# Optimization experiments

Measured on AMD Instinct MI355X. Metric: run time of the kernel, lower is better.

## Reference

```python
import jax, jax.numpy as jnp
import numpy as np

BN_EPS = 1e-5


def _batchnorm(x, gamma, beta):
    # training-mode BatchNorm2d: biased batch stats over (N, H, W)
    mean = jnp.mean(x, axis=(0, 2, 3), keepdims=True)
    var = jnp.var(x, axis=(0, 2, 3), keepdims=True)
    xn = (x - mean) * jax.lax.rsqrt(var + BN_EPS)
    return xn * gamma[None, :, None, None] + beta[None, :, None, None]


def _bin_weight(w):
    # BitConv2d_Robust: w_bin = sign(w) * mean(|w|) per output channel (STE in fwd is just the value)
    alpha = jnp.mean(jnp.abs(w), axis=(1, 2, 3), keepdims=True)
    return jax.lax.stop_gradient(jnp.sign(w) * alpha - w) + w


def _conv(x, w, b, pad):
    y = jax.lax.conv_general_dilated(
        x, w, window_strides=(1, 1), padding=[(pad, pad), (pad, pad)],
        dimension_numbers=('NCHW', 'OIHW', 'NCHW'))
    return y + b[None, :, None, None]


def setup_inputs() -> dict:
    key = jax.random.key(0)
    ks = jax.random.split(key, 14)
    B, Cin, Cout, T, H, W = 16, 128, 256, 512, 64, 64
    fan1 = Cin * 9
    fan2 = Cout * 9
    return {
        'x': jax.random.normal(ks[0], (B, Cin, H, W), jnp.float32),
        't': jax.random.normal(ks[1], (B, T), jnp.float32),
        'bn1_g': jnp.ones((Cin,), jnp.float32),
        'bn1_b': jnp.zeros((Cin,), jnp.float32),
        'w1': jax.random.normal(ks[2], (Cout, Cin, 3, 3), jnp.float32) / np.sqrt(fan1),
        'b1': jax.random.normal(ks[3], (Cout,), jnp.float32) * 0.01,
        'tW': jax.random.normal(ks[4], (Cout, T), jnp.float32) / np.sqrt(T),
        'tb': jax.random.normal(ks[5], (Cout,), jnp.float32) * 0.01,
        'bn2_g': jnp.ones((Cout,), jnp.float32),
        'bn2_b': jnp.zeros((Cout,), jnp.float32),
        'w2': jax.random.normal(ks[6], (Cout, Cout, 3, 3), jnp.float32) / np.sqrt(fan2),
        'b2': jax.random.normal(ks[7], (Cout,), jnp.float32) * 0.01,
        'ws': jax.random.normal(ks[8], (Cout, Cin, 1, 1), jnp.float32) / np.sqrt(Cin),
        'bs': jax.random.normal(ks[9], (Cout,), jnp.float32) * 0.01,
    }


def reference(x, t, bn1_g, bn1_b, w1, b1, tW, tb, bn2_g, bn2_b, w2, b2, ws, bs):
    h = jnp.sign(_batchnorm(x, bn1_g, bn1_b))                # BN + sign binarize
    h = _conv(h, _bin_weight(w1), b1, pad=1)                  # binarized 3x3 conv
    temb = t @ tW.T + tb                                      # time MLP -> [B, Cout]
    h = h + temb[:, :, None, None]
    h = jnp.sign(_batchnorm(h, bn2_g, bn2_b))
    h = _conv(h, _bin_weight(w2), b2, pad=1)
    skip = _conv(x, _bin_weight(ws), bs, pad=0)               # 1x1 binarized skip (in_ch != out_ch)
    return h + skip
```

## Files before the change

### kernel.cpp

```cpp
#include <hip/hip_runtime.h>
#include <stdint.h>

typedef unsigned int uint;
typedef short bf16x8 __attribute__((ext_vector_type(8)));
typedef float f32x4 __attribute__((ext_vector_type(4)));

#define EPS 1e-5f


__global__ __launch_bounds__(256) void k_bn1_part(const float* __restrict__ x, float* __restrict__ part) {
  int c = blockIdx.x, chunk = blockIdx.y;
  float s = 0.f, s2 = 0.f;
  #pragma unroll
  for (int jb = 0; jb < 2; ++jb) {
    int b = chunk * 2 + jb;
    const float4* xb = (const float4*)(x + (((size_t)((b << 7) | c)) << 12));
    #pragma unroll
    for (int k = 0; k < 4; ++k) {
      float4 q = xb[k * 256 + threadIdx.x];
      s += (q.x + q.y) + (q.z + q.w);
      s2 += q.x * q.x + q.y * q.y + q.z * q.z + q.w * q.w;
    }
  }
  #pragma unroll
  for (int off = 32; off > 0; off >>= 1) { s += __shfl_down(s, off); s2 += __shfl_down(s2, off); }
  __shared__ float ls[4], ls2[4];
  int wid = threadIdx.x >> 6, lane = threadIdx.x & 63;
  if (lane == 0) { ls[wid] = s; ls2[wid] = s2; }
  __syncthreads();
  if (threadIdx.x == 0) {
    part[(c * 8 + chunk) * 2 + 0] = ls[0] + ls[1] + ls[2] + ls[3];
    part[(c * 8 + chunk) * 2 + 1] = ls2[0] + ls2[1] + ls2[2] + ls2[3];
  }
}

__global__ void k_bn1_fin(const float* __restrict__ part, const float* __restrict__ g,
                          const float* __restrict__ be, float* __restrict__ sc, float* __restrict__ sh) {
  int c = threadIdx.x;
  float s = 0.f, s2 = 0.f;
  for (int k = 0; k < 8; ++k) { s += part[(c * 8 + k) * 2]; s2 += part[(c * 8 + k) * 2 + 1]; }
  const float inv = 1.f / 65536.f;
  float m = s * inv, var = s2 * inv - m * m;
  float rs = rsqrtf(var + EPS);
  float scale = rs * g[c];
  sc[c] = scale;
  sh[c] = be[c] - m * scale;
}

__global__ __launch_bounds__(128) void k_packw1(const float* __restrict__ w1, uint* __restrict__ wb,
                                                float* __restrict__ alpha) {
  int co = blockIdx.x, wid = threadIdx.x >> 6, lane = threadIdx.x & 63;
  const float* wp = w1 + (co * 128 + threadIdx.x) * 9;
  float wv[9]; float s = 0.f;
  #pragma unroll
  for (int tp = 0; tp < 9; ++tp) { wv[tp] = wp[tp]; s += fabsf(wv[tp]); }
  #pragma unroll
  for (int tp = 0; tp < 9; ++tp) {
    unsigned long long m = __ballot(wv[tp] > 0.f);
    if (lane == 0) {
      wb[(co * 9 + tp) * 4 + wid * 2 + 0] = (uint)m;
      wb[(co * 9 + tp) * 4 + wid * 2 + 1] = (uint)(m >> 32);
    }
  }
  #pragma unroll
  for (int off = 32; off > 0; off >>= 1) s += __shfl_down(s, off);
  __shared__ float l2[2];
  if (lane == 0) l2[wid] = s;
  __syncthreads();
  if (threadIdx.x == 0) alpha[co] = (l2[0] + l2[1]) * (1.f / 1152.f);
}

__global__ __launch_bounds__(256) void k_packw2(const float* __restrict__ w2, uint* __restrict__ wb,
                                                float* __restrict__ alpha, ushort* __restrict__ wT) {
  int co = blockIdx.x, wid = threadIdx.x >> 6, lane = threadIdx.x & 63;
  int ci = threadIdx.x;
  const float* wp = w2 + (co * 256 + ci) * 9;
  float wv[9]; float s = 0.f;
  #pragma unroll
  for (int tp = 0; tp < 9; ++tp) { wv[tp] = wp[tp]; s += fabsf(wv[tp]); }
  int chunk = ci >> 7, kc = (ci >> 5) & 3, cil = ci & 31;
  #pragma unroll
  for (int tp = 0; tp < 9; ++tp) {
    wT[(((tp << 3) + (chunk << 2) + kc) << 13) + (co << 5) + cil] = (wv[tp] > 0.f) ? 0x3F80u : 0xBF80u;
    unsigned long long m = __ballot(wv[tp] > 0.f);
    if (lane == 0) {
      wb[(co * 9 + tp) * 8 + wid * 2 + 0] = (uint)m;
      wb[(co * 9 + tp) * 8 + wid * 2 + 1] = (uint)(m >> 32);
    }
  }
  #pragma unroll
  for (int off = 32; off > 0; off >>= 1) s += __shfl_down(s, off);
  __shared__ float l4[4];
  if (lane == 0) l4[wid] = s;
  __syncthreads();
  if (threadIdx.x == 0) alpha[co] = (l4[0] + l4[1] + l4[2] + l4[3]) * (1.f / 2304.f);
}

__global__ __launch_bounds__(256) void k_base(const uint* __restrict__ wb1, const uint* __restrict__ wb2,
                                              int* __restrict__ base1, int* __restrict__ base2) {
  int co = threadIdx.x;
  int pc1[9], pc2[9];
  #pragma unroll
  for (int tp = 0; tp < 9; ++tp) {
    uint a = 0;
    #pragma unroll
    for (int k = 0; k < 4; ++k) a += __popc(wb1[co * 36 + tp * 4 + k]);
    pc1[tp] = (int)a;
    uint b = 0;
    #pragma unroll
    for (int k = 0; k < 8; ++k) b += __popc(wb2[co * 72 + tp * 8 + k]);
    pc2[tp] = (int)b;
  }
  #pragma unroll
  for (int pat = 0; pat < 9; ++pat) {
    int yt = pat / 3, xt = pat % 3;
    int b1v = 1152, b2v = 2304;
    #pragma unroll
    for (int tp = 0; tp < 9; ++tp) {
      int dy = tp / 3 - 1, dx = tp % 3 - 1;
      bool inv = (dy < 0 && yt == 0) || (dy > 0 && yt == 2) || (dx < 0 && xt == 0) || (dx > 0 && xt == 2);
      if (inv) { b1v -= 128 - 2 * pc1[tp]; b2v -= 256 - 2 * pc2[tp]; }
    }
    base1[pat * 256 + co] = b1v;
    base2[pat * 256 + co] = b2v;
  }
}

__global__ __launch_bounds__(128) void k_packws(const float* __restrict__ wsk, float* __restrict__ swT) {
  int co = blockIdx.x, ci = threadIdx.x;
  float v = wsk[co * 128 + ci];
  float s = fabsf(v);
  #pragma unroll
  for (int off = 32; off > 0; off >>= 1) s += __shfl_down(s, off);
  __shared__ float l2[2]; __shared__ float tot;
  int wid = threadIdx.x >> 6, lane = threadIdx.x & 63;
  if (lane == 0) l2[wid] = s;
  __syncthreads();
  if (threadIdx.x == 0) tot = (l2[0] + l2[1]) * (1.f / 128.f);
  __syncthreads();
  float a = tot;
  swT[ci * 256 + co] = (v > 0.f) ? a : -a;
}

__global__ __launch_bounds__(256) void k_temb(const float* __restrict__ t, const float* __restrict__ tW,
                                              const float* __restrict__ tbias, float* __restrict__ temb) {
  int b = blockIdx.x, co = threadIdx.x;
  const float* tr = t + b * 512;
  const float* wr = tW + co * 512;
  float a0 = 0, a1 = 0, a2 = 0, a3 = 0;
  #pragma unroll 8
  for (int k = 0; k < 512; k += 4) {
    a0 = fmaf(tr[k + 0], wr[k + 0], a0);
    a1 = fmaf(tr[k + 1], wr[k + 1], a1);
    a2 = fmaf(tr[k + 2], wr[k + 2], a2);
    a3 = fmaf(tr[k + 3], wr[k + 3], a3);
  }
  temb[b * 256 + co] = (a0 + a1) + (a2 + a3) + tbias[co];
}

__global__ __launch_bounds__(256, 2) void k_skip(const float* __restrict__ x, const float* __restrict__ swT,
                                                 const float* __restrict__ bsk, const float* __restrict__ b2,
                                                 const float* __restrict__ sc1, const float* __restrict__ sh1,
                                                 uint* __restrict__ sbinw, float* __restrict__ out) {
  __shared__ float xs[128 * 64];
  __shared__ float wsl[128 * 64];
  int g = blockIdx.x;
  int b = g >> 6;
  int px0 = (g & 63) << 6;
  int co0 = blockIdx.y << 6;
  int t = threadIdx.x;

  {
    const float* xb = x + ((size_t)(b << 7) << 12) + px0;
    float4* xs4 = (float4*)xs;
    #pragma unroll
    for (int k = 0; k < 8; ++k) {
      int idx = k * 256 + t;
      int ci = idx >> 4, f4 = idx & 15;
      xs4[idx] = *(const float4*)(xb + ((size_t)ci << 12) + (f4 << 2));
    }
  }
  {
    float4* ws4 = (float4*)wsl;
    #pragma unroll
    for (int k = 0; k < 8; ++k) {
      int idx = k * 256 + t;
      int ci = idx >> 4, f4 = idx & 15;
      ws4[idx] = *(const float4*)(swT + ci * 256 + co0 + (f4 << 2));
    }
  }
  __syncthreads();

  if (blockIdx.y == 0) {
    int px = t & 63, wd = t >> 6;
    int ci0 = wd << 5;
    uint acc = 0;
    #pragma unroll
    for (int i = 0; i < 32; ++i) {
      int ci = ci0 + i;
      float v = xs[ci * 64 + px];
      acc |= ((v * sc1[ci] + sh1[ci]) > 0.f ? 1u : 0u) << i;
    }
    sbinw[(((size_t)b << 12) | (px0 + px)) * 4 + wd] = acc;
  }

  int tx = t & 15, ty = t >> 4;
  const float4* xs4 = (const float4*)xs;
  const float4* ws4 = (const float4*)wsl;
  float4 acc0 = make_float4(0, 0, 0, 0), acc1 = acc0, acc2 = acc0, acc3 = acc0;
  #pragma unroll 4
  for (int ci = 0; ci < 128; ++ci) {
    float4 xv = xs4[ci * 16 + tx];
    float4 wv = ws4[ci * 16 + ty];
    acc0.x = fmaf(wv.x, xv.x, acc0.x); acc0.y = fmaf(wv.x, xv.y, acc0.y);
    acc0.z = fmaf(wv.x, xv.z, acc0.z); acc0.w = fmaf(wv.x, xv.w, acc0.w);
    acc1.x = fmaf(wv.y, xv.x, acc1.x); acc1.y = fmaf(wv.y, xv.y, acc1.y);
    acc1.z = fmaf(wv.y, xv.z, acc1.z); acc1.w = fmaf(wv.y, xv.w, acc1.w);
    acc2.x = fmaf(wv.z, xv.x, acc2.x); acc2.y = fmaf(wv.z, xv.y, acc2.y);
    acc2.z = fmaf(wv.z, xv.z, acc2.z); acc2.w = fmaf(wv.z, xv.w, acc2.w);
    acc3.x = fmaf(wv.w, xv.x, acc3.x); acc3.y = fmaf(wv.w, xv.y, acc3.y);
    acc3.z = fmaf(wv.w, xv.z, acc3.z); acc3.w = fmaf(wv.w, xv.w, acc3.w);
  }

  float* op = out + ((size_t)b << 20) + px0 + (tx << 2);
  int cob = co0 + (ty << 2);
  float4 r;
  r = acc0; { float bb = bsk[cob + 0] + b2[cob + 0]; r.x += bb; r.y += bb; r.z += bb; r.w += bb; }
  *(float4*)(op + (size_t)(cob + 0) * 4096) = r;
  r = acc1; { float bb = bsk[cob + 1] + b2[cob + 1]; r.x += bb; r.y += bb; r.z += bb; r.w += bb; }
  *(float4*)(op + (size_t)(cob + 1) * 4096) = r;
  r = acc2; { float bb = bsk[cob + 2] + b2[cob + 2]; r.x += bb; r.y += bb; r.z += bb; r.w += bb; }
  *(float4*)(op + (size_t)(cob + 2) * 4096) = r;
  r = acc3; { float bb = bsk[cob + 3] + b2[cob + 3]; r.x += bb; r.y += bb; r.z += bb; r.w += bb; }
  *(float4*)(op + (size_t)(cob + 3) * 4096) = r;
}

__global__ __launch_bounds__(256, 1) void k_conv1(const uint4* __restrict__ sbin, const uint* __restrict__ wb1,
                                                  const int* __restrict__ base1, short* __restrict__ S1) {
  __shared__ uint wlds[32 * 36];
  __shared__ int blds[9 * 32];
  int co0 = blockIdx.y << 5;
  #pragma unroll
  for (int k = 0; k < 4; ++k) wlds[k * 256 + threadIdx.x] = wb1[co0 * 36 + k * 256 + threadIdx.x];
  if (threadIdx.x < 128) wlds[1024 + threadIdx.x] = wb1[co0 * 36 + 1024 + threadIdx.x];
  #pragma unroll
  for (int k = 0; k < 2; ++k) {
    int idx = k * 256 + threadIdx.x;
    if (idx < 288) blds[idx] = base1[(idx >> 5) * 256 + co0 + (idx & 31)];
  }

  int bt = blockIdx.x;
  int b = bt >> 4;
  int y = ((bt & 15) << 2) | (threadIdx.x >> 6);
  int cx = threadIdx.x & 63;
  uint nb[9][4];
  #pragma unroll
  for (int dy = -1; dy <= 1; ++dy)
    #pragma unroll
    for (int dx = -1; dx <= 1; ++dx) {
      int tp = (dy + 1) * 3 + (dx + 1);
      int yy = y + dy, xx = cx + dx;
      bool v = ((unsigned)yy < 64u) && ((unsigned)xx < 64u);
      uint4 q = make_uint4(0, 0, 0, 0);
      if (v) q = sbin[(b << 12) | (yy << 6) | xx];
      nb[tp][0] = q.x; nb[tp][1] = q.y; nb[tp][2] = q.z; nb[tp][3] = q.w;
    }
  int pat = ((y == 0) ? 0 : ((y == 63) ? 6 : 3)) + ((cx == 0) ? 0 : ((cx == 63) ? 2 : 1));
  __syncthreads();

  int p = (y << 6) | cx;
  short* op = S1 + ((size_t)b << 20) + ((size_t)co0 << 12) + p;
  #pragma unroll 1
  for (int cc = 0; cc < 4; ++cc) {
    short accv[8];
    #pragma unroll
    for (int j = 0; j < 8; ++j) {
      int co_l = cc * 8 + j;
      const uint4* wp4 = (const uint4*)(wlds + co_l * 36);
      uint m0 = 0, m1 = 0, m2 = 0, m3 = 0;
      #pragma unroll
      for (int tp = 0; tp < 9; ++tp) {
        uint4 w4 = wp4[tp];
        m0 += __popc(nb[tp][0] ^ w4.x);
        m1 += __popc(nb[tp][1] ^ w4.y);
        m2 += __popc(nb[tp][2] ^ w4.z);
        m3 += __popc(nb[tp][3] ^ w4.w);
      }
      accv[j] = (short)(blds[pat * 32 + co_l] - 2 * (int)((m0 + m1) + (m2 + m3)));
    }
    #pragma unroll
    for (int j = 0; j < 8; ++j) op[(size_t)(cc * 8 + j) << 12] = accv[j];
  }
}

__global__ __launch_bounds__(256) void k_bn2_part(const short* __restrict__ S1, const float* __restrict__ al1,
                                                  const float* __restrict__ b1, const float* __restrict__ temb,
                                                  float* __restrict__ part) {
  int co = blockIdx.x, chunk = blockIdx.y;
  float a = al1[co], bb = b1[co];
  float s = 0.f, s2 = 0.f;
  #pragma unroll
  for (int jb = 0; jb < 2; ++jb) {
    int b = chunk * 2 + jb;
    float tb_ = bb + temb[(b << 8) | co];
    const uint4* sp = (const uint4*)(S1 + ((size_t)b << 20) + ((size_t)co << 12));
    #pragma unroll
    for (int k = 0; k < 2; ++k) {
      uint4 q = sp[k * 256 + threadIdx.x];
      uint ws[4] = {q.x, q.y, q.z, q.w};
      #pragma unroll
      for (int w = 0; w < 4; ++w) {
        float f0 = fmaf(a, (float)((short)(ws[w] & 0xffffu)), tb_);
        float f1 = fmaf(a, (float)((short)(ws[w] >> 16)), tb_);
        s += f0 + f1;
        s2 += f0 * f0 + f1 * f1;
      }
    }
  }
  #pragma unroll
  for (int off = 32; off > 0; off >>= 1) { s += __shfl_down(s, off); s2 += __shfl_down(s2, off); }
  __shared__ float ls[4], ls2[4];
  int wid = threadIdx.x >> 6, lane = threadIdx.x & 63;
  if (lane == 0) { ls[wid] = s; ls2[wid] = s2; }
  __syncthreads();
  if (threadIdx.x == 0) {
    part[(co * 8 + chunk) * 2 + 0] = ls[0] + ls[1] + ls[2] + ls[3];
    part[(co * 8 + chunk) * 2 + 1] = ls2[0] + ls2[1] + ls2[2] + ls2[3];
  }
}

__global__ void k_bn2_fin(const float* __restrict__ part, const float* __restrict__ al1,
                          const float* __restrict__ b1, const float* __restrict__ g2,
                          const float* __restrict__ be2, float* __restrict__ A,
                          float* __restrict__ Bc, float* __restrict__ Cc) {
  int co = threadIdx.x;
  float s = 0.f, s2 = 0.f;
  for (int k = 0; k < 8; ++k) { s += part[(co * 8 + k) * 2]; s2 += part[(co * 8 + k) * 2 + 1]; }
  const float inv = 1.f / 65536.f;
  float m = s * inv, var = s2 * inv - m * m;
  float rs = rsqrtf(var + EPS);
  float gg = rs * g2[co];
  A[co] = al1[co] * gg;
  Bc[co] = (b1[co] - m) * gg + be2[co];
  Cc[co] = gg;
}

__global__ __launch_bounds__(256) void k_bin2_bf16(const short* __restrict__ S1, const float* __restrict__ A,
                                                   const float* __restrict__ Bc, const float* __restrict__ Cc,
                                                   const float* __restrict__ temb, uint4* __restrict__ h2u4) {
  __shared__ uint4 tile[64 * 32];
  int b = blockIdx.x >> 6;
  int px0 = (blockIdx.x & 63) << 6;
  int pxl = threadIdx.x & 63, quad = threadIdx.x >> 6;
  const short* sp = S1 + ((size_t)b << 20) + (px0 + pxl);
  const float* tp = temb + (b << 8);
  #pragma unroll 1
  for (int g = 0; g < 8; ++g) {
    uint d[4];
    #pragma unroll
    for (int h = 0; h < 4; ++h) {
      int c0 = quad * 64 + g * 8 + h * 2;
      float v0 = A[c0] * (float)sp[(size_t)c0 << 12] + Bc[c0] + Cc[c0] * tp[c0];
      float v1 = A[c0 + 1] * (float)sp[(size_t)(c0 + 1) << 12] + Bc[c0 + 1] + Cc[c0 + 1] * tp[c0 + 1];
      uint s0 = (v0 > 0.f) ? 0x3F80u : 0xBF80u;
      uint s1 = (v1 > 0.f) ? 0x3F80u : 0xBF80u;
      d[h] = s0 | (s1 << 16);
    }
    int slot = quad * 8 + g;
    tile[pxl * 32 + (slot ^ (pxl & 7))] = make_uint4(d[0], d[1], d[2], d[3]);
  }
  __syncthreads();
  uint4* dst = h2u4 + ((size_t)(b << 12) + px0) * 32;
  #pragma unroll
  for (int k = 0; k < 8; ++k) {
    int c = k * 256 + threadIdx.x;
    int px = c >> 5, slot = c & 31;
    dst[c] = tile[px * 32 + (slot ^ (px & 7))];
  }
}

__global__ __launch_bounds__(256, 2) void k_conv2_mfma(const ushort* __restrict__ h2,
                                                       const ushort* __restrict__ wT,
                                                       const float* __restrict__ al2,
                                                       float* __restrict__ out) {
  __shared__ ushort act[4 * 66 * 128];
  int bidx = blockIdx.x;
  int s = (bidx & 7) * 64 + (bidx >> 3);
  int b = s >> 5, y0 = (s & 31) << 1;
  int lane = threadIdx.x & 63, wave = threadIdx.x >> 6;
  int co0 = wave << 6;
  int l15 = lane & 15, lk = lane >> 4;

  f32x4 acc[4][8] = {};

  const uint4* h2g = (const uint4*)h2;
  uint4* a4 = (uint4*)act;
  const size_t abase = (size_t)((co0 + l15) << 5) + (lk << 3);

#define LOADAV(dst, ptr)                                                     \
  {                                                                          \
    _Pragma("unroll")                                                        \
    for (int ct_ = 0; ct_ < 4; ++ct_)                                        \
      dst[ct_] = *(const bf16x8*)((ptr) + abase + (ct_ << 9));               \
  }

#define KC_BLOCK(AV, kcv)                                                    \
  {                                                                          \
    _Pragma("unroll")                                                        \
    for (int r_ = 0; r_ < 2; ++r_) {                                         \
      bf16x8 Bv[4];                                                          \
      _Pragma("unroll")                                                      \
      for (int pt_ = 0; pt_ < 4; ++pt_) {                                    \
        int xi_ = (r_ + ty) * 66 + tx + pt_ * 16 + l15;                      \
        int u_ = (((xi_ << 4) + ((kcv) << 2) + lk) ^ (xi_ & 7));             \
        Bv[pt_] = *(bf16x8*)&act[u_ << 3];                                   \
      }                                                                      \
      _Pragma("unroll")                                                      \
      for (int ct_ = 0; ct_ < 4; ++ct_)                                      \
        _Pragma("unroll")                                                    \
        for (int pt_ = 0; pt_ < 4; ++pt_)                                    \
          acc[ct_][r_ * 4 + pt_] = __builtin_amdgcn_mfma_f32_16x16x32_bf16(  \
              AV[ct_], Bv[pt_], acc[ct_][r_ * 4 + pt_], 0, 0, 0);            \
    }                                                                        \
  }

  #pragma unroll 1
  for (int chunk = 0; chunk < 2; ++chunk) {
    if (chunk) __syncthreads();
    #pragma unroll 1
    for (int i = 0; i < 17; ++i) {
      int idx = i * 256 + threadIdx.x;
      if (idx < 4224) {
        int q = idx & 15, rowxz = idx >> 4;
        int xz = rowxz % 66, r = rowxz / 66;
        int yy = y0 + r - 1, xx = xz - 1;
        uint4 v = make_uint4(0, 0, 0, 0);
        if (((unsigned)yy < 64u) && ((unsigned)xx < 64u))
          v = h2g[(size_t)((b << 12) | (yy << 6) | xx) * 32 + chunk * 16 + q];
        a4[((rowxz << 4) + q) ^ (rowxz & 7)] = v;
      }
    }
    __syncthreads();

    const ushort* wch = wT + ((size_t)chunk << 15);
    bf16x8 AvA[4], AvB[4];
    LOADAV(AvA, wch);

    #pragma unroll 1
    for (int tp = 0; tp < 9; ++tp) {
      int ty = tp / 3, tx = tp % 3;
      const ushort* wtp = wch + ((size_t)tp << 16);
      const ushort* wnx = (tp < 8) ? (wtp + (1 << 16)) : wtp;

      LOADAV(AvB, wtp + (1 << 13));  KC_BLOCK(AvA, 0);
      LOADAV(AvA, wtp + (2 << 13));  KC_BLOCK(AvB, 1);
      LOADAV(AvB, wtp + (3 << 13));  KC_BLOCK(AvA, 2);
      LOADAV(AvA, wnx);              KC_BLOCK(AvB, 3);
    }
  }
#undef LOADAV
#undef KC_BLOCK

  #pragma unroll
  for (int ct = 0; ct < 4; ++ct) {
    #pragma unroll
    for (int r = 0; r < 2; ++r) {
      #pragma unroll
      for (int pt = 0; pt < 4; ++pt) {
        int x = pt * 16 + l15;
        float* ob = out + ((size_t)b << 20) + ((y0 + r) << 6) + x;
        #pragma unroll
        for (int j = 0; j < 4; ++j) {
          int co = co0 + ct * 16 + lk * 4 + j;
          float* p = ob + ((size_t)co << 12);
          *p = fmaf(al2[co], acc[ct][r * 4 + pt][j], *p);
        }
      }
    }
  }
}

__global__ __launch_bounds__(256) void k_bin2_packed(const short* __restrict__ S1, const float* __restrict__ A,
                                                     const float* __restrict__ Bc, const float* __restrict__ Cc,
                                                     const float* __restrict__ temb, uint4* __restrict__ hbin) {
  int pg = blockIdx.x * 256 + threadIdx.x;
  int b = pg >> 12, p = pg & 4095;
  int c0 = blockIdx.y << 7;
  const short* sp = S1 + ((size_t)b << 20) + p;
  const float* tp = temb + (b << 8);
  uint w[4];
  #pragma unroll
  for (int wd = 0; wd < 4; ++wd) {
    uint acc = 0;
    #pragma unroll
    for (int i = 0; i < 32; ++i) {
      int co = c0 + wd * 32 + i;
      float v = A[co] * (float)sp[(size_t)co << 12] + Bc[co] + Cc[co] * tp[co];
      acc |= (v > 0.f ? 1u : 0u) << i;
    }
    w[wd] = acc;
  }
  hbin[pg * 2 + blockIdx.y] = make_uint4(w[0], w[1], w[2], w[3]);
}

__global__ __launch_bounds__(256, 1) void k_conv2_pop(const uint4* __restrict__ hbin, const uint* __restrict__ wb2,
                                                      const int* __restrict__ base2, const float* __restrict__ al2,
                                                      float* __restrict__ out) {
  __shared__ uint wlds[32 * 72];
  __shared__ int blds[9 * 32];
  int co0 = blockIdx.y << 5;
  #pragma unroll
  for (int k = 0; k < 9; ++k) wlds[k * 256 + threadIdx.x] = wb2[co0 * 72 + k * 256 + threadIdx.x];
  #pragma unroll
  for (int k = 0; k < 2; ++k) {
    int idx = k * 256 + threadIdx.x;
    if (idx < 288) blds[idx] = base2[(idx >> 5) * 256 + co0 + (idx & 31)];
  }
  int bt = blockIdx.x;
  int b = bt >> 4;
  int y = ((bt & 15) << 2) | (threadIdx.x >> 6);
  int cx = threadIdx.x & 63;
  uint nb[9][8];
  #pragma unroll
  for (int dy = -1; dy <= 1; ++dy)
    #pragma unroll
    for (int dx = -1; dx <= 1; ++dx) {
      int tp = (dy + 1) * 3 + (dx + 1);
      int yy = y + dy, xx = cx + dx;
      bool v = ((unsigned)yy < 64u) && ((unsigned)xx < 64u);
      uint4 q0 = make_uint4(0, 0, 0, 0), q1 = make_uint4(0, 0, 0, 0);
      if (v) {
        int pix = (b << 12) | (yy << 6) | xx;
        q0 = hbin[pix * 2 + 0];
        q1 = hbin[pix * 2 + 1];
      }
      nb[tp][0] = q0.x; nb[tp][1] = q0.y; nb[tp][2] = q0.z; nb[tp][3] = q0.w;
      nb[tp][4] = q1.x; nb[tp][5] = q1.y; nb[tp][6] = q1.z; nb[tp][7] = q1.w;
    }
  int pat = ((y == 0) ? 0 : ((y == 63) ? 6 : 3)) + ((cx == 0) ? 0 : ((cx == 63) ? 2 : 1));
  __syncthreads();

  int p = (y << 6) | cx;
  float* op = out + ((size_t)b << 20) + ((size_t)co0 << 12) + p;
  #pragma unroll 1
  for (int cc = 0; cc < 4; ++cc) {
    float ov[8];
    #pragma unroll
    for (int j = 0; j < 8; ++j) ov[j] = op[(size_t)(cc * 8 + j) << 12];
    #pragma unroll
    for (int j = 0; j < 8; ++j) {
      int co_l = cc * 8 + j;
      const uint4* wp4 = (const uint4*)(wlds + co_l * 72);
      uint m0 = 0, m1 = 0, m2 = 0, m3 = 0;
      #pragma unroll
      for (int tp = 0; tp < 9; ++tp) {
        uint4 wa = wp4[tp * 2 + 0];
        uint4 wb_ = wp4[tp * 2 + 1];
        m0 += __popc(nb[tp][0] ^ wa.x);
        m1 += __popc(nb[tp][1] ^ wa.y);
        m2 += __popc(nb[tp][2] ^ wa.z);
        m3 += __popc(nb[tp][3] ^ wa.w);
        m0 += __popc(nb[tp][4] ^ wb_.x);
        m1 += __popc(nb[tp][5] ^ wb_.y);
        m2 += __popc(nb[tp][6] ^ wb_.z);
        m3 += __popc(nb[tp][7] ^ wb_.w);
      }
      int acc = blds[pat * 32 + co_l] - 2 * (int)((m0 + m1) + (m2 + m3));
      ov[j] = fmaf(al2[co0 + co_l], (float)acc, ov[j]);
    }
    #pragma unroll
    for (int j = 0; j < 8; ++j) op[(size_t)(cc * 8 + j) << 12] = ov[j];
  }
}

extern "C" void kernel_launch(void* const* d_in, const int* in_sizes, int n_in,
                              void* d_out, int out_size, void* d_ws, size_t ws_size,
                              hipStream_t stream) {
  const float* x    = (const float*)d_in[0];
  const float* t    = (const float*)d_in[1];
  const float* bn1g = (const float*)d_in[2];
  const float* bn1b = (const float*)d_in[3];
  const float* w1   = (const float*)d_in[4];
  const float* b1   = (const float*)d_in[5];
  const float* tW   = (const float*)d_in[6];
  const float* tb   = (const float*)d_in[7];
  const float* bn2g = (const float*)d_in[8];
  const float* bn2b = (const float*)d_in[9];
  const float* w2   = (const float*)d_in[10];
  const float* b2   = (const float*)d_in[11];
  const float* wsk  = (const float*)d_in[12];
  const float* bsk  = (const float*)d_in[13];
  float* out = (float*)d_out;
  char* ws = (char*)d_ws;

  float* bn1part = (float*)(ws + 0);
  float* sc1     = (float*)(ws + 8192);
  float* sh1     = (float*)(ws + 8704);
  uint4* sbin    = (uint4*)(ws + 9216);
  uint*  wb1     = (uint*) (ws + 1057792);
  float* al1     = (float*)(ws + 1094656);
  uint*  wb2     = (uint*) (ws + 1095680);
  float* al2     = (float*)(ws + 1169408);
  float* swkT    = (float*)(ws + 1170432);
  float* temb    = (float*)(ws + 1301504);
  float* bn2part = (float*)(ws + 1317888);
  float* A2      = (float*)(ws + 1334272);
  float* Bc2     = (float*)(ws + 1335296);
  float* Cc2     = (float*)(ws + 1336320);
  int*   base1g  = (int*)  (ws + 1337344);
  int*   base2g  = (int*)  (ws + 1346560);
  uint4* hbin    = (uint4*)(ws + 1355776);
  ushort* wT2    = (ushort*)(ws + 3452928);
  short* S1      = (short*)(ws + 4632576);
  ushort* h2     = (ushort*)(ws + 38187008);
  const size_t WS_NEED_MFMA = 71741440ULL;
  bool use_mfma = (ws_size >= WS_NEED_MFMA);

  k_bn1_part<<<dim3(128, 8), 256, 0, stream>>>(x, bn1part);
  k_bn1_fin<<<1, 128, 0, stream>>>(bn1part, bn1g, bn1b, sc1, sh1);
  k_packw1<<<256, 128, 0, stream>>>(w1, wb1, al1);
  k_packw2<<<256, 256, 0, stream>>>(w2, wb2, al2, wT2);
  k_base<<<1, 256, 0, stream>>>(wb1, wb2, base1g, base2g);
  k_packws<<<256, 128, 0, stream>>>(wsk, swkT);
  k_temb<<<16, 256, 0, stream>>>(t, tW, tb, temb);
  k_skip<<<dim3(1024, 4), 256, 0, stream>>>(x, swkT, bsk, b2, sc1, sh1, (uint*)sbin, out);
  k_conv1<<<dim3(256, 8), 256, 0, stream>>>(sbin, wb1, base1g, S1);
  k_bn2_part<<<dim3(256, 8), 256, 0, stream>>>(S1, al1, b1, temb, bn2part);
  k_bn2_fin<<<1, 256, 0, stream>>>(bn2part, al1, b1, bn2g, bn2b, A2, Bc2, Cc2);
  if (use_mfma) {
    k_bin2_bf16<<<1024, 256, 0, stream>>>(S1, A2, Bc2, Cc2, temb, (uint4*)h2);
    k_conv2_mfma<<<512, 256, 0, stream>>>(h2, wT2, al2, out);
  } else {
    k_bin2_packed<<<dim3(256, 2), 256, 0, stream>>>(S1, A2, Bc2, Cc2, temb, hbin);
    k_conv2_pop<<<dim3(256, 8), 256, 0, stream>>>(hbin, wb2, base2g, al2, out);
  }
}
```

Baseline: 240.2 us.

## Run conv1 on bf16 MFMA with fused BN2 partial statistics

```diff
diff --git a/kernel.cpp b/kernel.cpp
--- a/kernel.cpp
+++ b/kernel.cpp
@@ -48,14 +48,16 @@
 }
 
 __global__ __launch_bounds__(128) void k_packw1(const float* __restrict__ w1, uint* __restrict__ wb,
-                                                float* __restrict__ alpha) {
+                                                float* __restrict__ alpha, ushort* __restrict__ wT1) {
   int co = blockIdx.x, wid = threadIdx.x >> 6, lane = threadIdx.x & 63;
-  const float* wp = w1 + (co * 128 + threadIdx.x) * 9;
+  int ci = threadIdx.x;
+  const float* wp = w1 + (co * 128 + ci) * 9;
   float wv[9]; float s = 0.f;
   #pragma unroll
   for (int tp = 0; tp < 9; ++tp) { wv[tp] = wp[tp]; s += fabsf(wv[tp]); }
   #pragma unroll
   for (int tp = 0; tp < 9; ++tp) {
+    wT1[(((tp << 2) + (ci >> 5)) << 13) + (co << 5) + (ci & 31)] = (wv[tp] > 0.f) ? 0x3F80u : 0xBF80u;
     unsigned long long m = __ballot(wv[tp] > 0.f);
     if (lane == 0) {
       wb[(co * 9 + tp) * 4 + wid * 2 + 0] = (uint)m;
@@ -161,7 +163,8 @@
 __global__ __launch_bounds__(256, 2) void k_skip(const float* __restrict__ x, const float* __restrict__ swT,
                                                  const float* __restrict__ bsk, const float* __restrict__ b2,
                                                  const float* __restrict__ sc1, const float* __restrict__ sh1,
-                                                 uint* __restrict__ sbinw, float* __restrict__ out) {
+                                                 uint* __restrict__ sbinw, ushort* __restrict__ h1w,
+                                                 int mfma1, float* __restrict__ out) {
   __shared__ float xs[128 * 64];
   __shared__ float wsl[128 * 64];
   int g = blockIdx.x;
@@ -194,14 +197,27 @@
   if (blockIdx.y == 0) {
     int px = t & 63, wd = t >> 6;
     int ci0 = wd << 5;
-    uint acc = 0;
-    #pragma unroll
-    for (int i = 0; i < 32; ++i) {
-      int ci = ci0 + i;
-      float v = xs[ci * 64 + px];
-      acc |= ((v * sc1[ci] + sh1[ci]) > 0.f ? 1u : 0u) << i;
-    }
-    sbinw[(((size_t)b << 12) | (px0 + px)) * 4 + wd] = acc;
+    if (mfma1) {
+      ushort hv[32];
+      #pragma unroll
+      for (int i = 0; i < 32; ++i) {
+        int ci = ci0 + i;
+        float v = xs[ci * 64 + px];
+        hv[i] = ((v * sc1[ci] + sh1[ci]) > 0.f) ? (ushort)0x3F80u : (ushort)0xBF80u;
+      }
+      uint4* dst = (uint4*)(h1w + (((size_t)((b << 12) | (px0 + px))) << 7) + (wd << 5));
+      const uint4* src = (const uint4*)hv;
+      dst[0] = src[0]; dst[1] = src[1]; dst[2] = src[2]; dst[3] = src[3];
+    } else {
+      uint acc = 0;
+      #pragma unroll
+      for (int i = 0; i < 32; ++i) {
+        int ci = ci0 + i;
+        float v = xs[ci * 64 + px];
+        acc |= ((v * sc1[ci] + sh1[ci]) > 0.f ? 1u : 0u) << i;
+      }
+      sbinw[(((size_t)b << 12) | (px0 + px)) * 4 + wd] = acc;
+    }
   }
 
   int tx = t & 15, ty = t >> 4;
@@ -235,154 +251,11 @@
   *(float4*)(op + (size_t)(cob + 3) * 4096) = r;
 }
 
-__global__ __launch_bounds__(256, 1) void k_conv1(const uint4* __restrict__ sbin, const uint* __restrict__ wb1,
-                                                  const int* __restrict__ base1, short* __restrict__ S1) {
-  __shared__ uint wlds[32 * 36];
-  __shared__ int blds[9 * 32];
-  int co0 = blockIdx.y << 5;
-  #pragma unroll
-  for (int k = 0; k < 4; ++k) wlds[k * 256 + threadIdx.x] = wb1[co0 * 36 + k * 256 + threadIdx.x];
-  if (threadIdx.x < 128) wlds[1024 + threadIdx.x] = wb1[co0 * 36 + 1024 + threadIdx.x];
-  #pragma unroll
-  for (int k = 0; k < 2; ++k) {
-    int idx = k * 256 + threadIdx.x;
-    if (idx < 288) blds[idx] = base1[(idx >> 5) * 256 + co0 + (idx & 31)];
-  }
-
-  int bt = blockIdx.x;
-  int b = bt >> 4;
-  int y = ((bt & 15) << 2) | (threadIdx.x >> 6);
-  int cx = threadIdx.x & 63;
-  uint nb[9][4];
-  #pragma unroll
-  for (int dy = -1; dy <= 1; ++dy)
-    #pragma unroll
-    for (int dx = -1; dx <= 1; ++dx) {
-      int tp = (dy + 1) * 3 + (dx + 1);
-      int yy = y + dy, xx = cx + dx;
-      bool v = ((unsigned)yy < 64u) && ((unsigned)xx < 64u);
-      uint4 q = make_uint4(0, 0, 0, 0);
-      if (v) q = sbin[(b << 12) | (yy << 6) | xx];
-      nb[tp][0] = q.x; nb[tp][1] = q.y; nb[tp][2] = q.z; nb[tp][3] = q.w;
-    }
-  int pat = ((y == 0) ? 0 : ((y == 63) ? 6 : 3)) + ((cx == 0) ? 0 : ((cx == 63) ? 2 : 1));
-  __syncthreads();
-
-  int p = (y << 6) | cx;
-  short* op = S1 + ((size_t)b << 20) + ((size_t)co0 << 12) + p;
-  #pragma unroll 1
-  for (int cc = 0; cc < 4; ++cc) {
-    short accv[8];
-    #pragma unroll
-    for (int j = 0; j < 8; ++j) {
-      int co_l = cc * 8 + j;
-      const uint4* wp4 = (const uint4*)(wlds + co_l * 36);
-      uint m0 = 0, m1 = 0, m2 = 0, m3 = 0;
-      #pragma unroll
-      for (int tp = 0; tp < 9; ++tp) {
-        uint4 w4 = wp4[tp];
-        m0 += __popc(nb[tp][0] ^ w4.x);
-        m1 += __popc(nb[tp][1] ^ w4.y);
-        m2 += __popc(nb[tp][2] ^ w4.z);
-        m3 += __popc(nb[tp][3] ^ w4.w);
-      }
-      accv[j] = (short)(blds[pat * 32 + co_l] - 2 * (int)((m0 + m1) + (m2 + m3)));
-    }
-    #pragma unroll
-    for (int j = 0; j < 8; ++j) op[(size_t)(cc * 8 + j) << 12] = accv[j];
-  }
-}
-
-__global__ __launch_bounds__(256) void k_bn2_part(const short* __restrict__ S1, const float* __restrict__ al1,
-                                                  const float* __restrict__ b1, const float* __restrict__ temb,
-                                                  float* __restrict__ part) {
-  int co = blockIdx.x, chunk = blockIdx.y;
-  float a = al1[co], bb = b1[co];
-  float s = 0.f, s2 = 0.f;
-  #pragma unroll
-  for (int jb = 0; jb < 2; ++jb) {
-    int b = chunk * 2 + jb;
-    float tb_ = bb + temb[(b << 8) | co];
-    const uint4* sp = (const uint4*)(S1 + ((size_t)b << 20) + ((size_t)co << 12));
-    #pragma unroll
-    for (int k = 0; k < 2; ++k) {
-      uint4 q = sp[k * 256 + threadIdx.x];
-      uint ws[4] = {q.x, q.y, q.z, q.w};
-      #pragma unroll
-      for (int w = 0; w < 4; ++w) {
-        float f0 = fmaf(a, (float)((short)(ws[w] & 0xffffu)), tb_);
-        float f1 = fmaf(a, (float)((short)(ws[w] >> 16)), tb_);
-        s += f0 + f1;
-        s2 += f0 * f0 + f1 * f1;
-      }
-    }
-  }
-  #pragma unroll
-  for (int off = 32; off > 0; off >>= 1) { s += __shfl_down(s, off); s2 += __shfl_down(s2, off); }
-  __shared__ float ls[4], ls2[4];
-  int wid = threadIdx.x >> 6, lane = threadIdx.x & 63;
-  if (lane == 0) { ls[wid] = s; ls2[wid] = s2; }
-  __syncthreads();
-  if (threadIdx.x == 0) {
-    part[(co * 8 + chunk) * 2 + 0] = ls[0] + ls[1] + ls[2] + ls[3];
-    part[(co * 8 + chunk) * 2 + 1] = ls2[0] + ls2[1] + ls2[2] + ls2[3];
-  }
-}
-
-__global__ void k_bn2_fin(const float* __restrict__ part, const float* __restrict__ al1,
-                          const float* __restrict__ b1, const float* __restrict__ g2,
-                          const float* __restrict__ be2, float* __restrict__ A,
-                          float* __restrict__ Bc, float* __restrict__ Cc) {
-  int co = threadIdx.x;
-  float s = 0.f, s2 = 0.f;
-  for (int k = 0; k < 8; ++k) { s += part[(co * 8 + k) * 2]; s2 += part[(co * 8 + k) * 2 + 1]; }
-  const float inv = 1.f / 65536.f;
-  float m = s * inv, var = s2 * inv - m * m;
-  float rs = rsqrtf(var + EPS);
-  float gg = rs * g2[co];
-  A[co] = al1[co] * gg;
-  Bc[co] = (b1[co] - m) * gg + be2[co];
-  Cc[co] = gg;
-}
-
-__global__ __launch_bounds__(256) void k_bin2_bf16(const short* __restrict__ S1, const float* __restrict__ A,
-                                                   const float* __restrict__ Bc, const float* __restrict__ Cc,
-                                                   const float* __restrict__ temb, uint4* __restrict__ h2u4) {
-  __shared__ uint4 tile[64 * 32];
-  int b = blockIdx.x >> 6;
-  int px0 = (blockIdx.x & 63) << 6;
-  int pxl = threadIdx.x & 63, quad = threadIdx.x >> 6;
-  const short* sp = S1 + ((size_t)b << 20) + (px0 + pxl);
-  const float* tp = temb + (b << 8);
-  #pragma unroll 1
-  for (int g = 0; g < 8; ++g) {
-    uint d[4];
-    #pragma unroll
-    for (int h = 0; h < 4; ++h) {
-      int c0 = quad * 64 + g * 8 + h * 2;
-      float v0 = A[c0] * (float)sp[(size_t)c0 << 12] + Bc[c0] + Cc[c0] * tp[c0];
-      float v1 = A[c0 + 1] * (float)sp[(size_t)(c0 + 1) << 12] + Bc[c0 + 1] + Cc[c0 + 1] * tp[c0 + 1];
-      uint s0 = (v0 > 0.f) ? 0x3F80u : 0xBF80u;
-      uint s1 = (v1 > 0.f) ? 0x3F80u : 0xBF80u;
-      d[h] = s0 | (s1 << 16);
-    }
-    int slot = quad * 8 + g;
-    tile[pxl * 32 + (slot ^ (pxl & 7))] = make_uint4(d[0], d[1], d[2], d[3]);
-  }
-  __syncthreads();
-  uint4* dst = h2u4 + ((size_t)(b << 12) + px0) * 32;
-  #pragma unroll
-  for (int k = 0; k < 8; ++k) {
-    int c = k * 256 + threadIdx.x;
-    int px = c >> 5, slot = c & 31;
-    dst[c] = tile[px * 32 + (slot ^ (px & 7))];
-  }
-}
-
-__global__ __launch_bounds__(256, 2) void k_conv2_mfma(const ushort* __restrict__ h2,
-                                                       const ushort* __restrict__ wT,
-                                                       const float* __restrict__ al2,
-                                                       float* __restrict__ out) {
+__global__ __launch_bounds__(256, 2) void k_conv1_mfma(const ushort* __restrict__ h1,
+                                                       const ushort* __restrict__ wT1,
+                                                       short* __restrict__ S1,
+                                                       float* __restrict__ part_s,
+                                                       float* __restrict__ part_s2) {
   __shared__ ushort act[4 * 66 * 128];
   int bidx = blockIdx.x;
   int s = (bidx & 7) * 64 + (bidx >> 3);
@@ -392,8 +265,7 @@
   int l15 = lane & 15, lk = lane >> 4;
 
   f32x4 acc[4][8] = {};
-
-  const uint4* h2g = (const uint4*)h2;
+  const uint4* h1g = (const uint4*)h1;
   uint4* a4 = (uint4*)act;
   const size_t abase = (size_t)((co0 + l15) << 5) + (lk << 3);
 
@@ -403,7 +275,6 @@
     for (int ct_ = 0; ct_ < 4; ++ct_)                                        \
       dst[ct_] = *(const bf16x8*)((ptr) + abase + (ct_ << 9));               \
   }
-
 #define KC_BLOCK(AV, kcv)                                                    \
   {                                                                          \
     _Pragma("unroll")                                                        \
@@ -425,6 +296,299 @@
   }
 
   #pragma unroll 1
+  for (int i = 0; i < 17; ++i) {
+    int idx = i * 256 + threadIdx.x;
+    if (idx < 4224) {
+      int q = idx & 15, rowxz = idx >> 4;
+      int xz = rowxz % 66, r = rowxz / 66;
+      int yy = y0 + r - 1, xx = xz - 1;
+      uint4 v = make_uint4(0, 0, 0, 0);
+      if (((unsigned)yy < 64u) && ((unsigned)xx < 64u))
+        v = h1g[(size_t)((b << 12) | (yy << 6) | xx) * 16 + q];
+      a4[((rowxz << 4) + q) ^ (rowxz & 7)] = v;
+    }
+  }
+  __syncthreads();
+
+  bf16x8 AvA[4], AvB[4];
+  LOADAV(AvA, wT1);
+  #pragma unroll 1
+  for (int tp = 0; tp < 9; ++tp) {
+    int ty = tp / 3, tx = tp % 3;
+    const ushort* wtp = wT1 + ((size_t)tp << 15);
+    const ushort* wnx = (tp < 8) ? (wtp + (1 << 15)) : wtp;
+
+    LOADAV(AvB, wtp + (1 << 13));  KC_BLOCK(AvA, 0);
+    LOADAV(AvA, wtp + (2 << 13));  KC_BLOCK(AvB, 1);
+    LOADAV(AvB, wtp + (3 << 13));  KC_BLOCK(AvA, 2);
+    LOADAV(AvA, wnx);              KC_BLOCK(AvB, 3);
+  }
+#undef LOADAV
+#undef KC_BLOCK
+
+  #pragma unroll
+  for (int ct = 0; ct < 4; ++ct)
+    #pragma unroll
+    for (int r = 0; r < 2; ++r)
+      #pragma unroll
+      for (int pt = 0; pt < 4; ++pt) {
+        int x = pt * 16 + l15;
+        short* ob = S1 + ((size_t)b << 20) + ((y0 + r) << 6) + x;
+        #pragma unroll
+        for (int j = 0; j < 4; ++j) {
+          int co = co0 + ct * 16 + lk * 4 + j;
+          ob[(size_t)co << 12] = (short)acc[ct][r * 4 + pt][j];
+        }
+      }
+  #pragma unroll
+  for (int ct = 0; ct < 4; ++ct) {
+    float s1v[4] = {0, 0, 0, 0}, s2v[4] = {0, 0, 0, 0};
+    #pragma unroll
+    for (int k = 0; k < 8; ++k)
+      #pragma unroll
+      for (int j = 0; j < 4; ++j) {
+        float v = acc[ct][k][j];
+        s1v[j] += v; s2v[j] += v * v;
+      }
+    #pragma unroll
+    for (int off = 1; off < 16; off <<= 1)
+      #pragma unroll
+      for (int j = 0; j < 4; ++j) {
+        s1v[j] += __shfl_xor(s1v[j], off);
+        s2v[j] += __shfl_xor(s2v[j], off);
+      }
+    if (l15 == 0) {
+      #pragma unroll
+      for (int j = 0; j < 4; ++j) {
+        int co = co0 + ct * 16 + lk * 4 + j;
+        part_s[(size_t)s * 256 + co] = s1v[j];
+        part_s2[(size_t)s * 256 + co] = s2v[j];
+      }
+    }
+  }
+}
+
+__global__ void k_bn2_fin2(const float* __restrict__ part_s, const float* __restrict__ part_s2,
+                           const float* __restrict__ al1, const float* __restrict__ b1,
+                           const float* __restrict__ g2, const float* __restrict__ be2,
+                           const float* __restrict__ temb,
+                           float* __restrict__ A, float* __restrict__ Bc, float* __restrict__ Cc) {
+  int co = blockIdx.x;
+  int t = threadIdx.x;
+  float sS = 0.f, scS = 0.f, s2 = 0.f;
+  for (int k = 0; k < 8; ++k) {
+    int blk = t + k * 64;
+    int b = blk >> 5;
+    float c = b1[co] + temb[(b << 8) + co];
+    float Sv = part_s[(size_t)blk * 256 + co];
+    sS += Sv; scS += c * Sv; s2 += part_s2[(size_t)blk * 256 + co];
+  }
+  #pragma unroll
+  for (int off = 32; off > 0; off >>= 1) {
+    sS += __shfl_down(sS, off); scS += __shfl_down(scS, off); s2 += __shfl_down(s2, off);
+  }
+  if (t == 0) {
+    float a = al1[co];
+    float sumc = 0.f, sumc2 = 0.f;
+    for (int b = 0; b < 16; ++b) { float c = b1[co] + temb[(b << 8) + co]; sumc += c; sumc2 += c * c; }
+    float sumY = a * sS + 4096.f * sumc;
+    float sumY2 = a * a * s2 + 2.f * a * scS + 4096.f * sumc2;
+    const float inv = 1.f / 65536.f;
+    float m = sumY * inv, var = sumY2 * inv - m * m;
+    float rs = rsqrtf(var + EPS);
+    float gg = rs * g2[co];
+    A[co] = a * gg;
+    Bc[co] = (b1[co] - m) * gg + be2[co];
+    Cc[co] = gg;
+  }
+}
+
+__global__ __launch_bounds__(256, 1) void k_conv1(const uint4* __restrict__ sbin, const uint* __restrict__ wb1,
+                                                  const int* __restrict__ base1, short* __restrict__ S1) {
+  __shared__ uint wlds[32 * 36];
+  __shared__ int blds[9 * 32];
+  int co0 = blockIdx.y << 5;
+  #pragma unroll
+  for (int k = 0; k < 4; ++k) wlds[k * 256 + threadIdx.x] = wb1[co0 * 36 + k * 256 + threadIdx.x];
+  if (threadIdx.x < 128) wlds[1024 + threadIdx.x] = wb1[co0 * 36 + 1024 + threadIdx.x];
+  #pragma unroll
+  for (int k = 0; k < 2; ++k) {
+    int idx = k * 256 + threadIdx.x;
+    if (idx < 288) blds[idx] = base1[(idx >> 5) * 256 + co0 + (idx & 31)];
+  }
+  int bt = blockIdx.x;
+  int b = bt >> 4;
+  int y = ((bt & 15) << 2) | (threadIdx.x >> 6);
+  int cx = threadIdx.x & 63;
+  uint nb[9][4];
+  #pragma unroll
+  for (int dy = -1; dy <= 1; ++dy)
+    #pragma unroll
+    for (int dx = -1; dx <= 1; ++dx) {
+      int tp = (dy + 1) * 3 + (dx + 1);
+      int yy = y + dy, xx = cx + dx;
+      bool v = ((unsigned)yy < 64u) && ((unsigned)xx < 64u);
+      uint4 q = make_uint4(0, 0, 0, 0);
+      if (v) q = sbin[(b << 12) | (yy << 6) | xx];
+      nb[tp][0] = q.x; nb[tp][1] = q.y; nb[tp][2] = q.z; nb[tp][3] = q.w;
+    }
+  int pat = ((y == 0) ? 0 : ((y == 63) ? 6 : 3)) + ((cx == 0) ? 0 : ((cx == 63) ? 2 : 1));
+  __syncthreads();
+  int p = (y << 6) | cx;
+  short* op = S1 + ((size_t)b << 20) + ((size_t)co0 << 12) + p;
+  #pragma unroll 1
+  for (int cc = 0; cc < 4; ++cc) {
+    short accv[8];
+    #pragma unroll
+    for (int j = 0; j < 8; ++j) {
+      int co_l = cc * 8 + j;
+      const uint4* wp4 = (const uint4*)(wlds + co_l * 36);
+      uint m0 = 0, m1 = 0, m2 = 0, m3 = 0;
+      #pragma unroll
+      for (int tp = 0; tp < 9; ++tp) {
+        uint4 w4 = wp4[tp];
+        m0 += __popc(nb[tp][0] ^ w4.x);
+        m1 += __popc(nb[tp][1] ^ w4.y);
+        m2 += __popc(nb[tp][2] ^ w4.z);
+        m3 += __popc(nb[tp][3] ^ w4.w);
+      }
+      accv[j] = (short)(blds[pat * 32 + co_l] - 2 * (int)((m0 + m1) + (m2 + m3)));
+    }
+    #pragma unroll
+    for (int j = 0; j < 8; ++j) op[(size_t)(cc * 8 + j) << 12] = accv[j];
+  }
+}
+
+__global__ __launch_bounds__(256) void k_bn2_part(const short* __restrict__ S1, const float* __restrict__ al1,
+                                                  const float* __restrict__ b1, const float* __restrict__ temb,
+                                                  float* __restrict__ part) {
+  int co = blockIdx.x, chunk = blockIdx.y;
+  float a = al1[co], bb = b1[co];
+  float s = 0.f, s2 = 0.f;
+  #pragma unroll
+  for (int jb = 0; jb < 2; ++jb) {
+    int b = chunk * 2 + jb;
+    float tb_ = bb + temb[(b << 8) | co];
+    const uint4* sp = (const uint4*)(S1 + ((size_t)b << 20) + ((size_t)co << 12));
+    #pragma unroll
+    for (int k = 0; k < 2; ++k) {
+      uint4 q = sp[k * 256 + threadIdx.x];
+      uint ws[4] = {q.x, q.y, q.z, q.w};
+      #pragma unroll
+      for (int w = 0; w < 4; ++w) {
+        float f0 = fmaf(a, (float)((short)(ws[w] & 0xffffu)), tb_);
+        float f1 = fmaf(a, (float)((short)(ws[w] >> 16)), tb_);
+        s += f0 + f1;
+        s2 += f0 * f0 + f1 * f1;
+      }
+    }
+  }
+  #pragma unroll
+  for (int off = 32; off > 0; off >>= 1) { s += __shfl_down(s, off); s2 += __shfl_down(s2, off); }
+  __shared__ float ls[4], ls2[4];
+  int wid = threadIdx.x >> 6, lane = threadIdx.x & 63;
+  if (lane == 0) { ls[wid] = s; ls2[wid] = s2; }
+  __syncthreads();
+  if (threadIdx.x == 0) {
+    part[(co * 8 + chunk) * 2 + 0] = ls[0] + ls[1] + ls[2] + ls[3];
+    part[(co * 8 + chunk) * 2 + 1] = ls2[0] + ls2[1] + ls2[2] + ls2[3];
+  }
+}
+
+__global__ void k_bn2_fin(const float* __restrict__ part, const float* __restrict__ al1,
+                          const float* __restrict__ b1, const float* __restrict__ g2,
+                          const float* __restrict__ be2, float* __restrict__ A,
+                          float* __restrict__ Bc, float* __restrict__ Cc) {
+  int co = threadIdx.x;
+  float s = 0.f, s2 = 0.f;
+  for (int k = 0; k < 8; ++k) { s += part[(co * 8 + k) * 2]; s2 += part[(co * 8 + k) * 2 + 1]; }
+  const float inv = 1.f / 65536.f;
+  float m = s * inv, var = s2 * inv - m * m;
+  float rs = rsqrtf(var + EPS);
+  float gg = rs * g2[co];
+  A[co] = al1[co] * gg;
+  Bc[co] = (b1[co] - m) * gg + be2[co];
+  Cc[co] = gg;
+}
+
+__global__ __launch_bounds__(256) void k_bin2_bf16(const short* __restrict__ S1, const float* __restrict__ A,
+                                                   const float* __restrict__ Bc, const float* __restrict__ Cc,
+                                                   const float* __restrict__ temb, uint4* __restrict__ h2u4) {
+  __shared__ uint4 tile[64 * 32];
+  int b = blockIdx.x >> 6;
+  int px0 = (blockIdx.x & 63) << 6;
+  int pxl = threadIdx.x & 63, quad = threadIdx.x >> 6;
+  const short* sp = S1 + ((size_t)b << 20) + (px0 + pxl);
+  const float* tp = temb + (b << 8);
+  #pragma unroll 1
+  for (int g = 0; g < 8; ++g) {
+    uint d[4];
+    #pragma unroll
+    for (int h = 0; h < 4; ++h) {
+      int c0 = quad * 64 + g * 8 + h * 2;
+      float v0 = A[c0] * (float)sp[(size_t)c0 << 12] + Bc[c0] + Cc[c0] * tp[c0];
+      float v1 = A[c0 + 1] * (float)sp[(size_t)(c0 + 1) << 12] + Bc[c0 + 1] + Cc[c0 + 1] * tp[c0 + 1];
+      uint s0 = (v0 > 0.f) ? 0x3F80u : 0xBF80u;
+      uint s1 = (v1 > 0.f) ? 0x3F80u : 0xBF80u;
+      d[h] = s0 | (s1 << 16);
+    }
+    int slot = quad * 8 + g;
+    tile[pxl * 32 + (slot ^ (pxl & 7))] = make_uint4(d[0], d[1], d[2], d[3]);
+  }
+  __syncthreads();
+  uint4* dst = h2u4 + ((size_t)(b << 12) + px0) * 32;
+  #pragma unroll
+  for (int k = 0; k < 8; ++k) {
+    int c = k * 256 + threadIdx.x;
+    int px = c >> 5, slot = c & 31;
+    dst[c] = tile[px * 32 + (slot ^ (px & 7))];
+  }
+}
+
+__global__ __launch_bounds__(256, 2) void k_conv2_mfma(const ushort* __restrict__ h2,
+                                                       const ushort* __restrict__ wT,
+                                                       const float* __restrict__ al2,
+                                                       float* __restrict__ out) {
+  __shared__ ushort act[4 * 66 * 128];
+  int bidx = blockIdx.x;
+  int s = (bidx & 7) * 64 + (bidx >> 3);
+  int b = s >> 5, y0 = (s & 31) << 1;
+  int lane = threadIdx.x & 63, wave = threadIdx.x >> 6;
+  int co0 = wave << 6;
+  int l15 = lane & 15, lk = lane >> 4;
+
+  f32x4 acc[4][8] = {};
+  const uint4* h2g = (const uint4*)h2;
+  uint4* a4 = (uint4*)act;
+  const size_t abase = (size_t)((co0 + l15) << 5) + (lk << 3);
+
+#define LOADAV(dst, ptr)                                                     \
+  {                                                                          \
+    _Pragma("unroll")                                                        \
+    for (int ct_ = 0; ct_ < 4; ++ct_)                                        \
+      dst[ct_] = *(const bf16x8*)((ptr) + abase + (ct_ << 9));               \
+  }
+#define KC_BLOCK(AV, kcv)                                                    \
+  {                                                                          \
+    _Pragma("unroll")                                                        \
+    for (int r_ = 0; r_ < 2; ++r_) {                                         \
+      bf16x8 Bv[4];                                                          \
+      _Pragma("unroll")                                                      \
+      for (int pt_ = 0; pt_ < 4; ++pt_) {                                    \
+        int xi_ = (r_ + ty) * 66 + tx + pt_ * 16 + l15;                      \
+        int u_ = (((xi_ << 4) + ((kcv) << 2) + lk) ^ (xi_ & 7));             \
+        Bv[pt_] = *(bf16x8*)&act[u_ << 3];                                   \
+      }                                                                      \
+      _Pragma("unroll")                                                      \
+      for (int ct_ = 0; ct_ < 4; ++ct_)                                      \
+        _Pragma("unroll")                                                    \
+        for (int pt_ = 0; pt_ < 4; ++pt_)                                    \
+          acc[ct_][r_ * 4 + pt_] = __builtin_amdgcn_mfma_f32_16x16x32_bf16(  \
+              AV[ct_], Bv[pt_], acc[ct_][r_ * 4 + pt_], 0, 0, 0);            \
+    }                                                                        \
+  }
+
+  #pragma unroll 1
   for (int chunk = 0; chunk < 2; ++chunk) {
     if (chunk) __syncthreads();
     #pragma unroll 1
@@ -539,7 +703,6 @@
     }
   int pat = ((y == 0) ? 0 : ((y == 63) ? 6 : 3)) + ((cx == 0) ? 0 : ((cx == 63) ? 2 : 1));
   __syncthreads();
-
   int p = (y << 6) | cx;
   float* op = out + ((size_t)b << 20) + ((size_t)co0 << 12) + p;
   #pragma unroll 1
@@ -609,25 +772,37 @@
   float* Cc2     = (float*)(ws + 1336320);
   int*   base1g  = (int*)  (ws + 1337344);
   int*   base2g  = (int*)  (ws + 1346560);
-  uint4* hbin    = (uint4*)(ws + 1355776);
-  ushort* wT2    = (ushort*)(ws + 3452928);
-  short* S1      = (short*)(ws + 4632576);
-  ushort* h2     = (ushort*)(ws + 38187008);
-  const size_t WS_NEED_MFMA = 71741440ULL;
-  bool use_mfma = (ws_size >= WS_NEED_MFMA);
+  uint4*  hbin    = (uint4*)(ws + 1355776);
+  float*  part_s  = (float*)(ws + 1355776);
+  float*  part_s2 = (float*)(ws + 1880064);
+  ushort* wT1     = (ushort*)(ws + 2404352);
+  ushort* wT2     = (ushort*)(ws + 3452928);
+  short*  S1      = (short*)(ws + 4632576);
+  ushort* h2      = (ushort*)(ws + 38187008);
+  ushort* h1      = (ushort*)(ws + 71741440);
+  const size_t WS_NEED2 = 71741440ULL;
+  const size_t WS_NEED1 = 88518656ULL;
+  bool mode2 = (ws_size >= WS_NEED2);
+  bool mode1 = (ws_size >= WS_NEED1);
 
   k_bn1_part<<<dim3(128, 8), 256, 0, stream>>>(x, bn1part);
   k_bn1_fin<<<1, 128, 0, stream>>>(bn1part, bn1g, bn1b, sc1, sh1);
-  k_packw1<<<256, 128, 0, stream>>>(w1, wb1, al1);
+  k_packw1<<<256, 128, 0, stream>>>(w1, wb1, al1, wT1);
   k_packw2<<<256, 256, 0, stream>>>(w2, wb2, al2, wT2);
   k_base<<<1, 256, 0, stream>>>(wb1, wb2, base1g, base2g);
   k_packws<<<256, 128, 0, stream>>>(wsk, swkT);
   k_temb<<<16, 256, 0, stream>>>(t, tW, tb, temb);
-  k_skip<<<dim3(1024, 4), 256, 0, stream>>>(x, swkT, bsk, b2, sc1, sh1, (uint*)sbin, out);
-  k_conv1<<<dim3(256, 8), 256, 0, stream>>>(sbin, wb1, base1g, S1);
-  k_bn2_part<<<dim3(256, 8), 256, 0, stream>>>(S1, al1, b1, temb, bn2part);
-  k_bn2_fin<<<1, 256, 0, stream>>>(bn2part, al1, b1, bn2g, bn2b, A2, Bc2, Cc2);
-  if (use_mfma) {
+  k_skip<<<dim3(1024, 4), 256, 0, stream>>>(x, swkT, bsk, b2, sc1, sh1, (uint*)sbin, h1,
+                                            mode1 ? 1 : 0, out);
+  if (mode1) {
+    k_conv1_mfma<<<512, 256, 0, stream>>>(h1, wT1, S1, part_s, part_s2);
+    k_bn2_fin2<<<256, 64, 0, stream>>>(part_s, part_s2, al1, b1, bn2g, bn2b, temb, A2, Bc2, Cc2);
+  } else {
+    k_conv1<<<dim3(256, 8), 256, 0, stream>>>(sbin, wb1, base1g, S1);
+    k_bn2_part<<<dim3(256, 8), 256, 0, stream>>>(S1, al1, b1, temb, bn2part);
+    k_bn2_fin<<<1, 256, 0, stream>>>(bn2part, al1, b1, bn2g, bn2b, A2, Bc2, Cc2);
+  }
+  if (mode2) {
     k_bin2_bf16<<<1024, 256, 0, stream>>>(S1, A2, Bc2, Cc2, temb, (uint4*)h2);
     k_conv2_mfma<<<512, 256, 0, stream>>>(h2, wT2, al2, out);
   } else {
```

Result: faster. 231.7 us (-3.5%).
